# Performance work log

Hardware: AMD Instinct MI355X
Metric: run time of the kernel (lower is better)

The kernel has to match this reference:

```python
import jax, jax.numpy as jnp
import numpy as np

N_AGENTS = 10
N_ENEMIES = 11
N_ALLIES = 9
H = 64           # rnn_hidden_dim
HYP = 64         # api_hyper_dim
DEPTH = 2        # residual_depth
OWN = 32
EF = 10          # enemy_feats_dim
AF = 10          # ally_feats_dim
N_ACTIONS = 17
BS = 1024


def _hypernet(x, win, bin_, wres, bres, wout, bout):
    # Linear -> ReLU -> DEPTH x (ReLU(Linear)+identity) -> Linear
    h = jax.nn.relu(x @ win + bin_)
    for d in range(DEPTH):
        h = jax.nn.relu(h @ wres[d] + bres[d]) + h
    return h @ wout + bout


def _gru_cell(x, h, wi, wh, bi, bh):
    gi = x @ wi + bi
    gh = h @ wh + bh
    ir, iz, in_ = jnp.split(gi, 3, axis=-1)
    hr, hz, hn = jnp.split(gh, 3, axis=-1)
    r = jax.nn.sigmoid(ir + hr)
    z = jax.nn.sigmoid(iz + hz)
    n = jnp.tanh(in_ + r * hn)
    return (1.0 - z) * n + z * h


def setup_inputs() -> dict:
    key = jax.random.key(0)
    ks = iter(jax.random.split(key, 48))
    def p(shape, s=0.1):
        return jax.random.normal(next(ks), shape, jnp.float32) * s
    N = BS * N_AGENTS
    inp = {
        'own_feats':    p((N, OWN), 1.0),
        'enemy_feats':  p((N * N_ENEMIES, EF), 1.0),
        'ally_feats':   p((N * N_ALLIES, AF), 1.0),
        'hidden_state': p((N, H), 1.0),
        'fc1_w': p((OWN, H)), 'fc1_b': p((H,)),
        'agent_emb': p((N_AGENTS, H)), 'action_emb': p((N_ACTIONS, H)),
        'hen_win': p((EF, HYP)), 'hen_bin': p((HYP,)),
        'hen_wres': p((DEPTH, HYP, HYP)), 'hen_bres': p((DEPTH, HYP)),
        'hen_wout': p((HYP, EF * H)), 'hen_bout': p((EF * H,)),
        'hal_win': p((AF, HYP)), 'hal_bin': p((HYP,)),
        'hal_wres': p((DEPTH, HYP, HYP)), 'hal_bres': p((DEPTH, HYP)),
        'hal_wout': p((HYP, AF * H)), 'hal_bout': p((AF * H,)),
        'gru_wi': p((H, 3 * H)), 'gru_wh': p((H, 3 * H)),
        'gru_bi': p((3 * H,)), 'gru_bh': p((3 * H,)),
        'fc2_w': p((H, 6)), 'fc2_b': p((6,)),
        'how_win': p((EF, HYP)), 'how_bin': p((HYP,)),
        'how_wres': p((DEPTH, HYP, HYP)), 'how_bres': p((DEPTH, HYP)),
        'how_wout': p((HYP, H)), 'how_bout': p((H,)),
        'hob_win': p((EF, HYP)), 'hob_bin': p((HYP,)),
        'hob_wres': p((DEPTH, HYP, HYP)), 'hob_bres': p((DEPTH, HYP)),
        'hob_wout': p((HYP, 1)), 'hob_bout': p((1,)),
        'agent_idx': jax.random.randint(next(ks), (N,), 0, N_AGENTS),
        'last_action_idx': jax.random.randint(next(ks), (N,), 0, N_ACTIONS),
        'bs': BS,
    }
    return inp


def reference(own_feats, enemy_feats, ally_feats, hidden_state,
              fc1_w, fc1_b, agent_emb, action_emb,
              hen_win, hen_bin, hen_wres, hen_bres, hen_wout, hen_bout,
              hal_win, hal_bin, hal_wres, hal_bres, hal_wout, hal_bout,
              gru_wi, gru_wh, gru_bi, gru_bh,
              fc2_w, fc2_b,
              how_win, how_bin, how_wres, how_bres, how_wout, how_bout,
              hob_win, hob_bin, hob_wres, hob_bres, hob_wout, hob_bout,
              agent_idx, last_action_idx, bs):
    N = bs * N_AGENTS
    # own embedding + id embeddings
    emb = own_feats @ fc1_w + fc1_b
    emb = emb + agent_emb[agent_idx] + action_emb[last_action_idx]
    # per-enemy hypernet weights [N*NE, EF, H]; bmm + sum-pool over enemies
    w_en = _hypernet(enemy_feats, hen_win, hen_bin, hen_wres, hen_bres,
                     hen_wout, hen_bout).reshape(-1, EF, H)
    emb_en = jnp.einsum('nf,nfh->nh', enemy_feats, w_en)
    emb_en = emb_en.reshape(N, N_ENEMIES, H).sum(axis=1)
    # per-ally hypernet weights + bmm + sum-pool
    w_al = _hypernet(ally_feats, hal_win, hal_bin, hal_wres, hal_bres,
                     hal_wout, hal_bout).reshape(-1, AF, H)
    emb_al = jnp.einsum('nf,nfh->nh', ally_feats, w_al)
    emb_al = emb_al.reshape(N, N_ALLIES, H).sum(axis=1)
    x = jax.nn.relu(emb + emb_en + emb_al)
    hh = _gru_cell(x, hidden_state.reshape(-1, H), gru_wi, gru_wh, gru_bi, gru_bh)
    q_normal = (hh @ fc2_w + fc2_b).reshape(bs, N_AGENTS, 6)
    # attack-action head: hypernet-generated per-enemy weights/biases
    ow = _hypernet(enemy_feats, how_win, how_bin, how_wres, how_bres,
                   how_wout, how_bout).reshape(N, N_ENEMIES, H)
    ob = _hypernet(enemy_feats, hob_win, hob_bin, hob_wres, hob_bres,
                   hob_wout, hob_bout).reshape(N, N_ENEMIES)
    q_attack = (jnp.einsum('nh,neh->ne', hh, ow) + ob).reshape(bs, N_AGENTS, N_ENEMIES)
    q = jnp.concatenate([q_normal, q_attack], axis=-1)
    return q, hh.reshape(bs, N_AGENTS, H)
```

## Files before the change

### kernel.cpp

```cpp
#include <hip/hip_runtime.h>

#define DI static __device__ __forceinline__

typedef short s16x8 __attribute__((ext_vector_type(8)));
typedef float f32x4 __attribute__((ext_vector_type(4)));
typedef float f32x2 __attribute__((ext_vector_type(2)));
typedef unsigned u32x2 __attribute__((ext_vector_type(2)));

DI unsigned short f2b(float f) {
  union { float f; unsigned u; } v; v.f = f;
  return (unsigned short)((v.u + 0x7FFF + ((v.u >> 16) & 1)) >> 16);
}
DI float b2f(unsigned short s) {
  union { unsigned u; float f; } v; v.u = ((unsigned)s) << 16;
  return v.f;
}
DI unsigned cvtpk(float lo, float hi) {
  unsigned r;
  asm("v_cvt_pk_bf16_f32 %0, %1, %2" : "=v"(r) : "v"(lo), "v"(hi));
  return r;
}
DI f32x4 MFMA(s16x8 a, s16x8 b, f32x4 c) {
  return __builtin_amdgcn_mfma_f32_16x16x32_bf16(a, b, c, 0, 0, 0);
}
DI s16x8 ldg8(const unsigned short* p) { return *(const s16x8*)p; }

#define OFF_WEN   0
#define OFF_WAL   10240
#define OFF_WHOW  20480
#define OFF_WHOB  30720
#define OFF_BGEN  40960
#define OFF_BGAL  83968
#define OFF_WIT   126976
#define OFF_WHT   139264
#define OFF_FC1T  151552
#define OFF_FC2E  153600
#define OFF_HOWT  154624
#define OFF_HOBT  158720
#define SH_END    159744
#define B_EMB_EN  (SH_END*2)
#define B_EMB_AL  (B_EMB_EN + 2621440)
#define B_HB      (B_EMB_AL + 2621440)
#define B_GBF     (B_HB + 40960)

#define XSTR 40
#define HSTR 72
#define PSTR 680

__global__ __launch_bounds__(256) void kprep(
    const float* __restrict__ hen_win, const float* __restrict__ hen_wres,
    const float* __restrict__ hal_win, const float* __restrict__ hal_wres,
    const float* __restrict__ how_win, const float* __restrict__ how_wres,
    const float* __restrict__ hob_win, const float* __restrict__ hob_wres,
    const float* __restrict__ hen_wout, const float* __restrict__ hen_bout,
    const float* __restrict__ hal_wout, const float* __restrict__ hal_bout,
    const float* __restrict__ gru_wi, const float* __restrict__ gru_wh,
    const float* __restrict__ fc1_w, const float* __restrict__ fc2_w,
    const float* __restrict__ how_bout, const float* __restrict__ how_wout,
    const float* __restrict__ hob_wout,
    unsigned short* __restrict__ ws)
{
  const int gid = blockIdx.x * 256 + threadIdx.x;
  const int gsz = gridDim.x * 256;
  for (int i = gid; i < 4 * 10240; i += gsz) {
    int s = i / 10240, idx = i - s * 10240;
    const float* win  = (s == 0) ? hen_win  : (s == 1) ? hal_win  : (s == 2) ? how_win  : hob_win;
    const float* wres = (s == 0) ? hen_wres : (s == 1) ? hal_wres : (s == 2) ? how_wres : hob_wres;
    float v;
    if (idx < 2048) { int n = idx >> 5, k = idx & 31; v = (k < 10) ? win[k*64 + n] : 0.f; }
    else { int r = idx - 2048; int d = r >> 12; int r2 = r & 4095; int n = r2 >> 6, k = r2 & 63;
           v = wres[d*4096 + k*64 + n]; }
    ws[s * 10240 + idx] = f2b(v);
  }
  for (int i = gid; i < 2 * 43008; i += gsz) {
    int s = i / 43008, idx = i - s * 43008;
    const float* wout = s ? hal_wout : hen_wout;
    const float* bout = s ? hal_bout : hen_bout;
    int kl = idx & 31, n = (idx >> 5) & 63, c = idx >> 11;
    int kfg = c * 32 + kl;
    float v = 0.f;
    if (kfg < 640)      { int k = kfg / 10, f = kfg - k * 10; v = wout[k*640 + f*64 + n]; }
    else if (kfg < 650) { v = bout[(kfg - 640)*64 + n]; }
    ws[(s ? OFF_BGAL : OFF_BGEN) + idx] = f2b(v);
  }
  for (int i = gid; i < 2 * 12288; i += gsz) {
    int s = i / 12288, idx = i - s * 12288;
    int n = idx >> 6, k = idx & 63;
    const float* w = s ? gru_wh : gru_wi;
    ws[(s ? OFF_WHT : OFF_WIT) + idx] = f2b(w[k*192 + n]);
  }
  for (int i = gid; i < 2048; i += gsz) { int n = i >> 5, k = i & 31; ws[OFF_FC1T + i] = f2b(fc1_w[k*64 + n]); }
  for (int i = gid; i < 1024; i += gsz) {
    int n = i >> 6, k = i & 63;
    float v = 0.f; if (n < 6) v = fc2_w[k*6 + n]; else if (n == 6) v = how_bout[k];
    ws[OFF_FC2E + i] = f2b(v);
  }
  for (int i = gid; i < 4096; i += gsz) ws[OFF_HOWT + i] = f2b(how_wout[i]);
}

template<int TMAX, bool WLAST>
DI void stack_batch(const unsigned short* __restrict__ x_lds,
                    unsigned short* const (&hbp)[TMAX], const int (&tis)[TMAX], int E,
                    const unsigned short* __restrict__ wg,
                    const float* __restrict__ bin, const float* __restrict__ bres,
                    f32x4 (&hval)[TMAX][4])
{
  const int l = threadIdx.x & 63;
  const int lrow = l & 15, gq = l >> 4, lk8 = gq * 8;
  {
    s16x8 wf[4]; f32x4 bv[4];
#pragma unroll
    for (int mt = 0; mt < 4; mt++) {
      wf[mt] = ldg8(wg + (mt*16 + lrow)*32 + lk8);
      bv[mt] = *(const f32x4*)(bin + mt*16 + gq*4);
    }
#pragma unroll
    for (int tt = 0; tt < TMAX; tt++) {
      if (tis[tt] < E) {
        s16x8 xf = *(const s16x8*)&x_lds[(tis[tt]*16 + lrow)*XSTR + lk8];
#pragma unroll
        for (int mt = 0; mt < 4; mt++) {
          f32x4 d = MFMA(wf[mt], xf, f32x4{0.f,0.f,0.f,0.f});
#pragma unroll
          for (int r = 0; r < 4; r++) hval[tt][mt][r] = fmaxf(d[r] + bv[mt][r], 0.f);
        }
        unsigned short* wr = hbp[tt] + lrow*HSTR;
#pragma unroll
        for (int mt = 0; mt < 4; mt++) {
          u32x2 pw;
          pw.x = cvtpk(hval[tt][mt][0], hval[tt][mt][1]);
          pw.y = cvtpk(hval[tt][mt][2], hval[tt][mt][3]);
          *(u32x2*)&wr[mt*16 + gq*4] = pw;
        }
      }
    }
  }
#pragma unroll
  for (int d = 0; d < 2; d++) {
    const unsigned short* wt = wg + 2048 + d * 4096;
    s16x8 wf[4][2]; f32x4 bv[4];
#pragma unroll
    for (int mt = 0; mt < 4; mt++) {
      wf[mt][0] = ldg8(wt + (mt*16 + lrow)*64 + lk8);
      wf[mt][1] = ldg8(wt + (mt*16 + lrow)*64 + 32 + lk8);
      bv[mt] = *(const f32x4*)(bres + d*64 + mt*16 + gq*4);
    }
#pragma unroll
    for (int tt = 0; tt < TMAX; tt++) {
      if (tis[tt] < E) {
        const unsigned short* hr = hbp[tt] + lrow*HSTR;
        s16x8 b0 = *(const s16x8*)&hr[lk8];
        s16x8 b1 = *(const s16x8*)&hr[32 + lk8];
#pragma unroll
        for (int mt = 0; mt < 4; mt++) {
          f32x4 a = MFMA(wf[mt][0], b0, f32x4{0.f,0.f,0.f,0.f});
          a = MFMA(wf[mt][1], b1, a);
#pragma unroll
          for (int r = 0; r < 4; r++)
            hval[tt][mt][r] = fmaxf(a[r] + bv[mt][r], 0.f) + hval[tt][mt][r];
        }
        if (d == 0 || WLAST) {
          unsigned short* wr = hbp[tt] + lrow*HSTR;
#pragma unroll
          for (int mt = 0; mt < 4; mt++) {
            u32x2 pw;
            pw.x = cvtpk(hval[tt][mt][0], hval[tt][mt][1]);
            pw.y = cvtpk(hval[tt][mt][2], hval[tt][mt][3]);
            *(u32x2*)&wr[mt*16 + gq*4] = pw;
          }
        }
      }
    }
  }
}

template<int E>
DI void hyp_body16(const float* __restrict__ feats,
                   const unsigned short* __restrict__ Wg, const unsigned short* __restrict__ Bg,
                   const float* __restrict__ bin, const float* __restrict__ bres,
                   float* __restrict__ emb, char* smem)
{
  unsigned short* x_lds = (unsigned short*)smem;
  unsigned short* h_lds = (unsigned short*)(smem + 14080);
  unsigned short* P     = (unsigned short*)smem;
  const int t = threadIdx.x;
  const int l = t & 63, wv = t >> 6;
  const int lrow = l & 15, gq = l >> 4, lk8 = gq * 8, lr4 = gq * 4;

  for (int idx = t; idx < E * 512; idx += 256) {
    int row = idx >> 5, c = idx & 31;
    x_lds[row*XSTR + c] = (c < 10) ? f2b(feats[row*10 + c]) : (unsigned short)0;
  }
  __syncthreads();

  int tis[3] = {wv, wv + 4, wv + 8};
  unsigned short* hbp[3] = { h_lds + (wv)*16*HSTR, h_lds + (wv+4)*16*HSTR, h_lds + (wv+8)*16*HSTR };
  f32x4 hval[3][4];
  stack_batch<3, true>(x_lds, hbp, tis, E, Wg, bin, bres, hval);
  __syncthreads();

  const int a = t >> 4, kq = t & 15, k0 = kq * 4;
  float acc[4][10];
#pragma unroll
  for (int kk = 0; kk < 4; kk++)
#pragma unroll
    for (int f = 0; f < 10; f++) acc[kk][f] = 0.f;
#pragma unroll
  for (int e = 0; e < E; e++) {
    int row = a * E + e;
    const unsigned short* xr = x_lds + row * XSTR;
    s16x8 xv8 = *(const s16x8*)xr;
    unsigned xv2 = *(const unsigned*)(xr + 8);
    float xf[10];
#pragma unroll
    for (int f = 0; f < 8; f++) xf[f] = b2f((unsigned short)xv8[f]);
    xf[8] = b2f((unsigned short)(xv2 & 0xFFFF));
    xf[9] = b2f((unsigned short)(xv2 >> 16));
    u32x2 hp = *(const u32x2*)&h_lds[row*HSTR + k0];
    float hf[4] = { b2f((unsigned short)(hp.x & 0xFFFF)), b2f((unsigned short)(hp.x >> 16)),
                    b2f((unsigned short)(hp.y & 0xFFFF)), b2f((unsigned short)(hp.y >> 16)) };
#pragma unroll
    for (int kk = 0; kk < 4; kk++)
#pragma unroll
      for (int f = 0; f < 10; f++) acc[kk][f] += hf[kk] * xf[f];
  }
  float sxv = 0.f; int a2 = 0, fx = 0;
  if (t < 160) {
    a2 = t / 10; fx = t - a2 * 10;
    for (int e = 0; e < E; e++) sxv += feats[(a2*E + e)*10 + fx];
  }
  __syncthreads();

  u32x2* Pw = (u32x2*)(P + a*PSTR + k0*10);
#pragma unroll
  for (int m = 0; m < 10; m++) {
    const int s0 = 4*m, s1 = 4*m+1, s2 = 4*m+2, s3 = 4*m+3;
    u32x2 pw;
    pw.x = cvtpk(acc[s0/10][s0%10], acc[s1/10][s1%10]);
    pw.y = cvtpk(acc[s2/10][s2%10], acc[s3/10][s3%10]);
    Pw[m] = pw;
  }
  if (t < 160) P[a2*PSTR + 640 + fx] = f2b(sxv);
  for (int i = t; i < 352; i += 256) { int a3 = i / 22, c = i - a3*22; P[a3*PSTR + 650 + c] = 0; }
  __syncthreads();

  f32x4 acc0 = {0.f,0.f,0.f,0.f}, acc1 = {0.f,0.f,0.f,0.f};
  const unsigned short* Bw = Bg + (wv*16 + lrow)*32 + lk8;
#pragma unroll
  for (int c = 0; c < 21; c++) {
    s16x8 af = *(const s16x8*)&P[lrow*PSTR + c*32 + lk8];
    s16x8 bf = ldg8(Bw + c*2048);
    if (c & 1) acc1 = MFMA(af, bf, acc1); else acc0 = MFMA(af, bf, acc0);
  }
#pragma unroll
  for (int r = 0; r < 4; r++)
    emb[(lr4 + r)*64 + wv*16 + lrow] = acc0[r] + acc1[r];
}

__global__ __launch_bounds__(256) void khyp_ea(
    const float* __restrict__ en_feats, const float* __restrict__ al_feats,
    const unsigned short* __restrict__ ws,
    const float* __restrict__ en_bin, const float* __restrict__ en_bres,
    const float* __restrict__ al_bin, const float* __restrict__ al_bres,
    float* __restrict__ emb_en, float* __restrict__ emb_al)
{
  __shared__ __align__(16) char smem[39424];
  if (blockIdx.x < 640) {
    int blk = blockIdx.x;
    hyp_body16<11>(en_feats + (long)blk*1760, ws + OFF_WEN, ws + OFF_BGEN,
                   en_bin, en_bres, emb_en + (long)blk*1024, smem);
  } else {
    int blk = blockIdx.x - 640;
    hyp_body16<9>(al_feats + (long)blk*1440, ws + OFF_WAL, ws + OFF_BGAL,
                  al_bin, al_bres, emb_al + (long)blk*1024, smem);
  }
}

__global__ __launch_bounds__(256) void kfused(
    const float* __restrict__ own, const float* __restrict__ agent_emb,
    const float* __restrict__ action_emb,
    const int* __restrict__ agent_idx, const int* __restrict__ last_action,
    const float* __restrict__ emb_en, const float* __restrict__ emb_al,
    const float* __restrict__ hidden,
    const unsigned short* __restrict__ ws,
    const float* __restrict__ fc1_b, const float* __restrict__ bi,
    const float* __restrict__ bh, const float* __restrict__ fc2_b,
    float* __restrict__ qout, float* __restrict__ hhout,
    unsigned short* __restrict__ g_bf, float* __restrict__ hb)
{
  __shared__ unsigned short own_lds[16*32];
  __shared__ unsigned short x_lds[16*HSTR];
  __shared__ unsigned short hp_lds[16*HSTR];
  __shared__ unsigned short hh_lds[16*HSTR];
  const int t = threadIdx.x;
  const int l = t & 63, wv = t >> 6;
  const int lrow = l & 15, lk8 = (l >> 4) * 8, lr4 = (l >> 4) * 4;
  const int n0 = blockIdx.x * 16;

  const unsigned short* fc1T = ws + OFF_FC1T;
  const unsigned short* wiT  = ws + OFF_WIT;
  const unsigned short* whT  = ws + OFF_WHT;
  const unsigned short* howT = ws + OFF_HOWT;
  const unsigned short* fc2e = ws + OFF_FC2E;

  for (int i = t; i < 512; i += 256) own_lds[i] = f2b(own[n0*32 + i]);
  for (int i = t; i < 1024; i += 256) hp_lds[(i >> 6)*HSTR + (i & 63)] = f2b(hidden[n0*64 + i]);
  __syncthreads();

  const int j = wv * 16 + lrow;
  {
    s16x8 a0 = *(const s16x8*)&own_lds[lrow*32 + lk8];
    s16x8 b0 = ldg8(fc1T + (wv*16 + lrow)*32 + lk8);
    f32x4 c0 = MFMA(a0, b0, f32x4{0.f,0.f,0.f,0.f});
    float fb = fc1_b[j];
#pragma unroll
    for (int r = 0; r < 4; r++) {
      int aa = lr4 + r; int n = n0 + aa;
      int ai = agent_idx[n], la = last_action[n];
      float v = c0[r] + fb + agent_emb[ai*64 + j] + action_emb[la*64 + j]
              + emb_en[n*64 + j] + emb_al[n*64 + j];
      x_lds[aa*HSTR + j] = f2b(fmaxf(v, 0.f));
    }
  }
  __syncthreads();

  {
    s16x8 xa[2], ha[2];
#pragma unroll
    for (int s = 0; s < 2; s++) {
      xa[s] = *(const s16x8*)&x_lds[lrow*HSTR + s*32 + lk8];
      ha[s] = *(const s16x8*)&hp_lds[lrow*HSTR + s*32 + lk8];
    }
    f32x4 gi[3], gh[3];
#pragma unroll
    for (int g3 = 0; g3 < 3; g3++) { gi[g3] = f32x4{0.f,0.f,0.f,0.f}; gh[g3] = f32x4{0.f,0.f,0.f,0.f}; }
#pragma unroll
    for (int g3 = 0; g3 < 3; g3++) {
      int tl = wv + g3 * 4;
#pragma unroll
      for (int s = 0; s < 2; s++) {
        gi[g3] = MFMA(xa[s], ldg8(wiT + (tl*16 + lrow)*64 + s*32 + lk8), gi[g3]);
        gh[g3] = MFMA(ha[s], ldg8(whT + (tl*16 + lrow)*64 + s*32 + lk8), gh[g3]);
      }
    }
    float bir = bi[j], biz = bi[64 + j], bin_ = bi[128 + j];
    float bhr = bh[j], bhz = bh[64 + j], bhn = bh[128 + j];
#pragma unroll
    for (int r = 0; r < 4; r++) {
      int aa = lr4 + r; int n = n0 + aa;
      float rr = 1.f / (1.f + __expf(-(gi[0][r] + bir + gh[0][r] + bhr)));
      float zz = 1.f / (1.f + __expf(-(gi[1][r] + biz + gh[1][r] + bhz)));
      float nn = tanhf(gi[2][r] + bin_ + rr * (gh[2][r] + bhn));
      float hp = hidden[n*64 + j];
      float hhv = (1.f - zz) * nn + zz * hp;
      hhout[n*64 + j] = hhv;
      hh_lds[aa*HSTR + j] = f2b(hhv);
    }
  }
  __syncthreads();

  {
    s16x8 hha[2];
#pragma unroll
    for (int s = 0; s < 2; s++) hha[s] = *(const s16x8*)&hh_lds[lrow*HSTR + s*32 + lk8];
    f32x4 gc = {0.f,0.f,0.f,0.f};
#pragma unroll
    for (int s = 0; s < 2; s++) gc = MFMA(hha[s], ldg8(howT + (wv*16 + lrow)*64 + s*32 + lk8), gc);
#pragma unroll
    for (int r = 0; r < 4; r++) g_bf[(n0 + lr4 + r)*64 + wv*16 + lrow] = f2b(gc[r]);
    if (wv == 0) {
      f32x4 qc = {0.f,0.f,0.f,0.f};
#pragma unroll
      for (int s = 0; s < 2; s++) qc = MFMA(hha[s], ldg8(fc2e + lrow*64 + s*32 + lk8), qc);
#pragma unroll
      for (int r = 0; r < 4; r++) {
        int n = n0 + lr4 + r;
        if (lrow < 6)       qout[n*17 + lrow] = qc[r] + fc2_b[lrow];
        else if (lrow == 6) hb[n] = qc[r];
      }
    }
  }
}

__global__ __launch_bounds__(256) void kattack(
    const float* __restrict__ en_feats, const unsigned short* __restrict__ ws,
    const float* __restrict__ how_bin, const float* __restrict__ how_bres,
    const float* __restrict__ hob_bin, const float* __restrict__ hob_bres,
    const unsigned short* __restrict__ g_bf, const float* __restrict__ hbuf,
    const float* __restrict__ hob_wout, const float* __restrict__ hob_bout,
    float* __restrict__ qout)
{
  __shared__ __align__(16) char smem[41728];
  unsigned short* x_lds = (unsigned short*)smem;
  unsigned short* scr   = (unsigned short*)(smem + 14080);
  const int t = threadIdx.x;
  const int l = t & 63, wv = t >> 6;
  const int lrow = l & 15, gq = l >> 4;
  const int blk = blockIdx.x;
  const float* feats = en_feats + (long)blk * 1760;

  for (int idx = t; idx < 176*32; idx += 256) {
    int row = idx >> 5, c = idx & 31;
    x_lds[row*XSTR + c] = (c < 10) ? f2b(feats[row*10 + c]) : (unsigned short)0;
  }
  __syncthreads();

  int tis[3] = {wv, wv + 4, wv + 8};
  unsigned short* hbp[3] = { scr + (wv*3+0)*16*HSTR, scr + (wv*3+1)*16*HSTR, scr + (wv*3+2)*16*HSTR };
  f32x4 hval[3][4];

  stack_batch<3, false>(x_lds, hbp, tis, 11, ws + OFF_WHOB, hob_bin, hob_bres, hval);
  f32x4 hw[4];
#pragma unroll
  for (int mt = 0; mt < 4; mt++) hw[mt] = *(const f32x4*)(hob_wout + mt*16 + gq*4);
  float qbv[3] = {0.f, 0.f, 0.f};
#pragma unroll
  for (int tt = 0; tt < 3; tt++) {
    if (tis[tt] < 11) {
      float s = 0.f;
#pragma unroll
      for (int mt = 0; mt < 4; mt++)
#pragma unroll
        for (int r = 0; r < 4; r++) s += hval[tt][mt][r] * hw[mt][r];
      s += __shfl_xor(s, 16, 64);
      s += __shfl_xor(s, 32, 64);
      qbv[tt] = s;
    }
  }

  stack_batch<3, false>(x_lds, hbp, tis, 11, ws + OFF_WHOW, how_bin, how_bres, hval);
  const float hob_b0 = hob_bout[0];
#pragma unroll
  for (int tt = 0; tt < 3; tt++) {
    if (tis[tt] < 11) {
      int row = tis[tt]*16 + lrow;
      int ag = (unsigned)row / 11u;
      int n = blk*16 + ag;
      float s = 0.f;
#pragma unroll
      for (int mt = 0; mt < 4; mt++) {
        u32x2 gv = *(const u32x2*)(g_bf + (long)n*64 + mt*16 + gq*4);
        s += hval[tt][mt][0] * b2f((unsigned short)(gv.x & 0xFFFF))
           + hval[tt][mt][1] * b2f((unsigned short)(gv.x >> 16))
           + hval[tt][mt][2] * b2f((unsigned short)(gv.y & 0xFFFF))
           + hval[tt][mt][3] * b2f((unsigned short)(gv.y >> 16));
      }
      s += __shfl_xor(s, 16, 64);
      s += __shfl_xor(s, 32, 64);
      if (l < 16) {
        int e = row - ag * 11;
        qout[n*17 + 6 + e] = s + qbv[tt] + hbuf[n] + hob_b0;
      }
    }
  }
}

extern "C" void kernel_launch(void* const* d_in, const int* in_sizes, int n_in,
                              void* d_out, int out_size, void* d_ws, size_t ws_size,
                              hipStream_t stream)
{
  (void)in_sizes; (void)n_in; (void)out_size; (void)ws_size;
  const float* own        = (const float*)d_in[0];
  const float* enemy      = (const float*)d_in[1];
  const float* ally       = (const float*)d_in[2];
  const float* hidden     = (const float*)d_in[3];
  const float* fc1_w      = (const float*)d_in[4];
  const float* fc1_b      = (const float*)d_in[5];
  const float* agent_emb  = (const float*)d_in[6];
  const float* action_emb = (const float*)d_in[7];
  const float* hen_win  = (const float*)d_in[8];  const float* hen_bin  = (const float*)d_in[9];
  const float* hen_wres = (const float*)d_in[10]; const float* hen_bres = (const float*)d_in[11];
  const float* hen_wout = (const float*)d_in[12]; const float* hen_bout = (const float*)d_in[13];
  const float* hal_win  = (const float*)d_in[14]; const float* hal_bin  = (const float*)d_in[15];
  const float* hal_wres = (const float*)d_in[16]; const float* hal_bres = (const float*)d_in[17];
  const float* hal_wout = (const float*)d_in[18]; const float* hal_bout = (const float*)d_in[19];
  const float* gru_wi = (const float*)d_in[20];   const float* gru_wh = (const float*)d_in[21];
  const float* gru_bi = (const float*)d_in[22];   const float* gru_bh = (const float*)d_in[23];
  const float* fc2_w  = (const float*)d_in[24];   const float* fc2_b  = (const float*)d_in[25];
  const float* how_win  = (const float*)d_in[26]; const float* how_bin  = (const float*)d_in[27];
  const float* how_wres = (const float*)d_in[28]; const float* how_bres = (const float*)d_in[29];
  const float* how_wout = (const float*)d_in[30]; const float* how_bout = (const float*)d_in[31];
  const float* hob_win  = (const float*)d_in[32]; const float* hob_bin  = (const float*)d_in[33];
  const float* hob_wres = (const float*)d_in[34]; const float* hob_bres = (const float*)d_in[35];
  const float* hob_wout = (const float*)d_in[36]; const float* hob_bout = (const float*)d_in[37];
  const int* agent_idx   = (const int*)d_in[38];
  const int* last_action = (const int*)d_in[39];

  unsigned short* ws = (unsigned short*)d_ws;
  float* emb_en = (float*)((char*)d_ws + B_EMB_EN);
  float* emb_al = (float*)((char*)d_ws + B_EMB_AL);
  float* hb     = (float*)((char*)d_ws + B_HB);
  unsigned short* g_bf = (unsigned short*)((char*)d_ws + B_GBF);

  float* q  = (float*)d_out;
  float* hh = q + 1024*10*17;

  kprep<<<128, 256, 0, stream>>>(hen_win, hen_wres, hal_win, hal_wres,
      how_win, how_wres, hob_win, hob_wres,
      hen_wout, hen_bout, hal_wout, hal_bout,
      gru_wi, gru_wh, fc1_w, fc2_w, how_bout, how_wout, hob_wout, ws);
  khyp_ea<<<1280, 256, 0, stream>>>(enemy, ally, ws,
      hen_bin, hen_bres, hal_bin, hal_bres, emb_en, emb_al);
  kfused<<<640, 256, 0, stream>>>(own, agent_emb, action_emb, agent_idx, last_action,
      emb_en, emb_al, hidden, ws, fc1_b, gru_bi, gru_bh, fc2_b, q, hh, g_bf, hb);
  kattack<<<640, 256, 0, stream>>>(enemy, ws, how_bin, how_bres, hob_bin, hob_bres,
      g_bf, hb, hob_wout, hob_bout, q);
}
```

Before: 78.49 us.

## Merge attack-head hypernet stacks into the hypernet kernel and fuse the attack dot-product into the GRU kernel

The attack-head hypernet stacks, which do not depend on the GRU output, now run inside the same launch as the enemy and ally hypernets. They write per-enemy bf16 hidden features and the bias term to workspace. The GRU kernel then computes the attack Q values with an MFMA against its locally held g vector in LDS, which removes the separate attack kernel and the g and hb round trips. The enemy and ally embeddings are also stored as bf16. In exchange this adds about 14 MB of hhow writes and reads plus some extra bf16 rounding, and the MFMA computes 16x16 outputs of which only the diagonal-matching ones are used.

```diff
diff --git a/kernel.cpp b/kernel.cpp
--- a/kernel.cpp
+++ b/kernel.cpp
@@ -4,7 +4,6 @@
 
 typedef short s16x8 __attribute__((ext_vector_type(8)));
 typedef float f32x4 __attribute__((ext_vector_type(4)));
-typedef float f32x2 __attribute__((ext_vector_type(2)));
 typedef unsigned u32x2 __attribute__((ext_vector_type(2)));
 
 DI unsigned short f2b(float f) {
@@ -36,12 +35,11 @@
 #define OFF_FC1T  151552
 #define OFF_FC2E  153600
 #define OFF_HOWT  154624
-#define OFF_HOBT  158720
 #define SH_END    159744
 #define B_EMB_EN  (SH_END*2)
-#define B_EMB_AL  (B_EMB_EN + 2621440)
-#define B_HB      (B_EMB_AL + 2621440)
-#define B_GBF     (B_HB + 40960)
+#define B_EMB_AL  (B_EMB_EN + 1310720)
+#define B_HHOW    (B_EMB_AL + 1310720)
+#define B_QB      (B_HHOW + 14417920)
 
 #define XSTR 40
 #define HSTR 72
@@ -57,7 +55,6 @@
     const float* __restrict__ gru_wi, const float* __restrict__ gru_wh,
     const float* __restrict__ fc1_w, const float* __restrict__ fc2_w,
     const float* __restrict__ how_bout, const float* __restrict__ how_wout,
-    const float* __restrict__ hob_wout,
     unsigned short* __restrict__ ws)
 {
   const int gid = blockIdx.x * 256 + threadIdx.x;
@@ -100,7 +97,7 @@
 
 template<int TMAX, bool WLAST>
 DI void stack_batch(const unsigned short* __restrict__ x_lds,
-                    unsigned short* const (&hbp)[TMAX], const int (&tis)[TMAX], int E,
+                    unsigned short* const (&hbp)[TMAX], const int (&tis)[TMAX], int NT,
                     const unsigned short* __restrict__ wg,
                     const float* __restrict__ bin, const float* __restrict__ bres,
                     f32x4 (&hval)[TMAX][4])
@@ -116,7 +113,7 @@
     }
 #pragma unroll
     for (int tt = 0; tt < TMAX; tt++) {
-      if (tis[tt] < E) {
+      if (tis[tt] < NT) {
         s16x8 xf = *(const s16x8*)&x_lds[(tis[tt]*16 + lrow)*XSTR + lk8];
 #pragma unroll
         for (int mt = 0; mt < 4; mt++) {
@@ -147,7 +144,7 @@
     }
 #pragma unroll
     for (int tt = 0; tt < TMAX; tt++) {
-      if (tis[tt] < E) {
+      if (tis[tt] < NT) {
         const unsigned short* hr = hbp[tt] + lrow*HSTR;
         s16x8 b0 = *(const s16x8*)&hr[lk8];
         s16x8 b1 = *(const s16x8*)&hr[32 + lk8];
@@ -178,7 +175,7 @@
 DI void hyp_body16(const float* __restrict__ feats,
                    const unsigned short* __restrict__ Wg, const unsigned short* __restrict__ Bg,
                    const float* __restrict__ bin, const float* __restrict__ bres,
-                   float* __restrict__ emb, char* smem)
+                   unsigned short* __restrict__ emb, char* smem)
 {
   unsigned short* x_lds = (unsigned short*)smem;
   unsigned short* h_lds = (unsigned short*)(smem + 14080);
@@ -254,47 +251,115 @@
   }
 #pragma unroll
   for (int r = 0; r < 4; r++)
-    emb[(lr4 + r)*64 + wv*16 + lrow] = acc0[r] + acc1[r];
-}
-
-__global__ __launch_bounds__(256) void khyp_ea(
+    emb[(lr4 + r)*64 + wv*16 + lrow] = f2b(acc0[r] + acc1[r]);
+}
+
+DI void attack_stacks(int blk, const float* __restrict__ en_feats,
+                      const unsigned short* __restrict__ ws,
+                      const float* __restrict__ how_bin, const float* __restrict__ how_bres,
+                      const float* __restrict__ hob_bin, const float* __restrict__ hob_bres,
+                      const float* __restrict__ hob_wout, float hob_b0,
+                      unsigned short* __restrict__ hhow, float* __restrict__ qB, char* smem)
+{
+  unsigned short* x_lds = (unsigned short*)smem;
+  unsigned short* scr   = (unsigned short*)(smem + 14080);
+  const int t = threadIdx.x;
+  const int l = t & 63, wv = t >> 6;
+  const int lrow = l & 15, gq = l >> 4;
+  const float* feats = en_feats + (long)blk * 1760;
+
+  for (int idx = t; idx < 176*32; idx += 256) {
+    int row = idx >> 5, c = idx & 31;
+    x_lds[row*XSTR + c] = (c < 10) ? f2b(feats[row*10 + c]) : (unsigned short)0;
+  }
+  __syncthreads();
+
+  int tis[3] = {wv, wv + 4, wv + 8};
+  unsigned short* hbp[3] = { scr + (wv*3+0)*16*HSTR, scr + (wv*3+1)*16*HSTR, scr + (wv*3+2)*16*HSTR };
+  f32x4 hval[3][4];
+
+  stack_batch<3, false>(x_lds, hbp, tis, 11, ws + OFF_WHOB, hob_bin, hob_bres, hval);
+  f32x4 hw[4];
+#pragma unroll
+  for (int mt = 0; mt < 4; mt++) hw[mt] = *(const f32x4*)(hob_wout + mt*16 + gq*4);
+#pragma unroll
+  for (int tt = 0; tt < 3; tt++) {
+    if (tis[tt] < 11) {
+      float s = 0.f;
+#pragma unroll
+      for (int mt = 0; mt < 4; mt++)
+#pragma unroll
+        for (int r = 0; r < 4; r++) s += hval[tt][mt][r] * hw[mt][r];
+      s += __shfl_xor(s, 16, 64);
+      s += __shfl_xor(s, 32, 64);
+      if (l < 16) qB[blk*176 + tis[tt]*16 + lrow] = s + hob_b0;
+    }
+  }
+
+  stack_batch<3, false>(x_lds, hbp, tis, 11, ws + OFF_WHOW, how_bin, how_bres, hval);
+#pragma unroll
+  for (int tt = 0; tt < 3; tt++) {
+    if (tis[tt] < 11) {
+      long row = (long)blk*176 + tis[tt]*16 + lrow;
+      unsigned short* wr = hhow + row*64;
+#pragma unroll
+      for (int mt = 0; mt < 4; mt++) {
+        u32x2 pw;
+        pw.x = cvtpk(hval[tt][mt][0], hval[tt][mt][1]);
+        pw.y = cvtpk(hval[tt][mt][2], hval[tt][mt][3]);
+        *(u32x2*)&wr[mt*16 + gq*4] = pw;
+      }
+    }
+  }
+}
+
+__global__ __launch_bounds__(256) void khyp_all(
     const float* __restrict__ en_feats, const float* __restrict__ al_feats,
     const unsigned short* __restrict__ ws,
     const float* __restrict__ en_bin, const float* __restrict__ en_bres,
     const float* __restrict__ al_bin, const float* __restrict__ al_bres,
-    float* __restrict__ emb_en, float* __restrict__ emb_al)
-{
-  __shared__ __align__(16) char smem[39424];
+    const float* __restrict__ how_bin, const float* __restrict__ how_bres,
+    const float* __restrict__ hob_bin, const float* __restrict__ hob_bres,
+    const float* __restrict__ hob_wout, const float* __restrict__ hob_bout,
+    unsigned short* __restrict__ emb_en, unsigned short* __restrict__ emb_al,
+    unsigned short* __restrict__ hhow, float* __restrict__ qB)
+{
+  __shared__ __align__(16) char smem[41728];
   if (blockIdx.x < 640) {
     int blk = blockIdx.x;
     hyp_body16<11>(en_feats + (long)blk*1760, ws + OFF_WEN, ws + OFF_BGEN,
                    en_bin, en_bres, emb_en + (long)blk*1024, smem);
-  } else {
+  } else if (blockIdx.x < 1280) {
     int blk = blockIdx.x - 640;
     hyp_body16<9>(al_feats + (long)blk*1440, ws + OFF_WAL, ws + OFF_BGAL,
                   al_bin, al_bres, emb_al + (long)blk*1024, smem);
-  }
-}
-
-__global__ __launch_bounds__(256) void kfused(
+  } else {
+    attack_stacks(blockIdx.x - 1280, en_feats, ws, how_bin, how_bres,
+                  hob_bin, hob_bres, hob_wout, hob_bout[0], hhow, qB, smem);
+  }
+}
+
+__global__ __launch_bounds__(256) void kfused2(
     const float* __restrict__ own, const float* __restrict__ agent_emb,
     const float* __restrict__ action_emb,
     const int* __restrict__ agent_idx, const int* __restrict__ last_action,
-    const float* __restrict__ emb_en, const float* __restrict__ emb_al,
+    const unsigned short* __restrict__ emb_en, const unsigned short* __restrict__ emb_al,
     const float* __restrict__ hidden,
     const unsigned short* __restrict__ ws,
     const float* __restrict__ fc1_b, const float* __restrict__ bi,
     const float* __restrict__ bh, const float* __restrict__ fc2_b,
-    float* __restrict__ qout, float* __restrict__ hhout,
-    unsigned short* __restrict__ g_bf, float* __restrict__ hb)
+    const unsigned short* __restrict__ hhow, const float* __restrict__ qB,
+    float* __restrict__ qout, float* __restrict__ hhout)
 {
   __shared__ unsigned short own_lds[16*32];
   __shared__ unsigned short x_lds[16*HSTR];
   __shared__ unsigned short hp_lds[16*HSTR];
   __shared__ unsigned short hh_lds[16*HSTR];
+  __shared__ unsigned short g_lds[16*HSTR];
+  __shared__ float hb_lds[16];
   const int t = threadIdx.x;
   const int l = t & 63, wv = t >> 6;
-  const int lrow = l & 15, lk8 = (l >> 4) * 8, lr4 = (l >> 4) * 4;
+  const int lrow = l & 15, gq = l >> 4, lk8 = gq * 8, lr4 = gq * 4;
   const int n0 = blockIdx.x * 16;
 
   const unsigned short* fc1T = ws + OFF_FC1T;
@@ -318,7 +383,7 @@
       int aa = lr4 + r; int n = n0 + aa;
       int ai = agent_idx[n], la = last_action[n];
       float v = c0[r] + fb + agent_emb[ai*64 + j] + action_emb[la*64 + j]
-              + emb_en[n*64 + j] + emb_al[n*64 + j];
+              + b2f(emb_en[(long)n*64 + j]) + b2f(emb_al[(long)n*64 + j]);
       x_lds[aa*HSTR + j] = f2b(fmaxf(v, 0.f));
     }
   }
@@ -367,7 +432,7 @@
 #pragma unroll
     for (int s = 0; s < 2; s++) gc = MFMA(hha[s], ldg8(howT + (wv*16 + lrow)*64 + s*32 + lk8), gc);
 #pragma unroll
-    for (int r = 0; r < 4; r++) g_bf[(n0 + lr4 + r)*64 + wv*16 + lrow] = f2b(gc[r]);
+    for (int r = 0; r < 4; r++) g_lds[(lr4 + r)*HSTR + wv*16 + lrow] = f2b(gc[r]);
     if (wv == 0) {
       f32x4 qc = {0.f,0.f,0.f,0.f};
 #pragma unroll
@@ -376,80 +441,35 @@
       for (int r = 0; r < 4; r++) {
         int n = n0 + lr4 + r;
         if (lrow < 6)       qout[n*17 + lrow] = qc[r] + fc2_b[lrow];
-        else if (lrow == 6) hb[n] = qc[r];
+        else if (lrow == 6) hb_lds[lr4 + r] = qc[r];
       }
     }
   }
-}
-
-__global__ __launch_bounds__(256) void kattack(
-    const float* __restrict__ en_feats, const unsigned short* __restrict__ ws,
-    const float* __restrict__ how_bin, const float* __restrict__ how_bres,
-    const float* __restrict__ hob_bin, const float* __restrict__ hob_bres,
-    const unsigned short* __restrict__ g_bf, const float* __restrict__ hbuf,
-    const float* __restrict__ hob_wout, const float* __restrict__ hob_bout,
-    float* __restrict__ qout)
-{
-  __shared__ __align__(16) char smem[41728];
-  unsigned short* x_lds = (unsigned short*)smem;
-  unsigned short* scr   = (unsigned short*)(smem + 14080);
-  const int t = threadIdx.x;
-  const int l = t & 63, wv = t >> 6;
-  const int lrow = l & 15, gq = l >> 4;
-  const int blk = blockIdx.x;
-  const float* feats = en_feats + (long)blk * 1760;
-
-  for (int idx = t; idx < 176*32; idx += 256) {
-    int row = idx >> 5, c = idx & 31;
-    x_lds[row*XSTR + c] = (c < 10) ? f2b(feats[row*10 + c]) : (unsigned short)0;
-  }
-  __syncthreads();
-
-  int tis[3] = {wv, wv + 4, wv + 8};
-  unsigned short* hbp[3] = { scr + (wv*3+0)*16*HSTR, scr + (wv*3+1)*16*HSTR, scr + (wv*3+2)*16*HSTR };
-  f32x4 hval[3][4];
-
-  stack_batch<3, false>(x_lds, hbp, tis, 11, ws + OFF_WHOB, hob_bin, hob_bres, hval);
-  f32x4 hw[4];
-#pragma unroll
-  for (int mt = 0; mt < 4; mt++) hw[mt] = *(const f32x4*)(hob_wout + mt*16 + gq*4);
-  float qbv[3] = {0.f, 0.f, 0.f};
-#pragma unroll
-  for (int tt = 0; tt < 3; tt++) {
-    if (tis[tt] < 11) {
-      float s = 0.f;
-#pragma unroll
-      for (int mt = 0; mt < 4; mt++)
-#pragma unroll
-        for (int r = 0; r < 4; r++) s += hval[tt][mt][r] * hw[mt][r];
-      s += __shfl_xor(s, 16, 64);
-      s += __shfl_xor(s, 32, 64);
-      qbv[tt] = s;
-    }
-  }
-
-  stack_batch<3, false>(x_lds, hbp, tis, 11, ws + OFF_WHOW, how_bin, how_bres, hval);
-  const float hob_b0 = hob_bout[0];
-#pragma unroll
-  for (int tt = 0; tt < 3; tt++) {
-    if (tis[tt] < 11) {
-      int row = tis[tt]*16 + lrow;
-      int ag = (unsigned)row / 11u;
-      int n = blk*16 + ag;
-      float s = 0.f;
-#pragma unroll
-      for (int mt = 0; mt < 4; mt++) {
-        u32x2 gv = *(const u32x2*)(g_bf + (long)n*64 + mt*16 + gq*4);
-        s += hval[tt][mt][0] * b2f((unsigned short)(gv.x & 0xFFFF))
-           + hval[tt][mt][1] * b2f((unsigned short)(gv.x >> 16))
-           + hval[tt][mt][2] * b2f((unsigned short)(gv.y & 0xFFFF))
-           + hval[tt][mt][3] * b2f((unsigned short)(gv.y >> 16));
-      }
-      s += __shfl_xor(s, 16, 64);
-      s += __shfl_xor(s, 32, 64);
-      if (l < 16) {
-        int e = row - ag * 11;
-        qout[n*17 + 6 + e] = s + qbv[tt] + hbuf[n] + hob_b0;
+  __syncthreads();
+
+  {
+    const long rb = (long)blockIdx.x * 176;
+#pragma unroll
+    for (int tt = 0; tt < 3; tt++) {
+      int ti = wv + tt * 4;
+      if (ti < 11) {
+        const unsigned short* hr = hhow + (rb + ti*16 + lrow)*64;
+        s16x8 af0 = ldg8(hr + lk8);
+        s16x8 af1 = ldg8(hr + 32 + lk8);
+        s16x8 bf0 = *(const s16x8*)&g_lds[lrow*HSTR + lk8];
+        s16x8 bf1 = *(const s16x8*)&g_lds[lrow*HSTR + 32 + lk8];
+        f32x4 c = MFMA(af0, bf0, f32x4{0.f,0.f,0.f,0.f});
+        c = MFMA(af1, bf1, c);
+#pragma unroll
+        for (int r = 0; r < 4; r++) {
+          int rowl = ti*16 + lr4 + r;
+          int ag = (unsigned)rowl / 11u;
+          if (ag == lrow) {
+            int e = rowl - ag * 11;
+            int n = n0 + ag;
+            qout[n*17 + 6 + e] = c[r] + qB[rb + rowl] + hb_lds[ag];
+          }
+        }
       }
     }
   }
@@ -487,10 +507,10 @@
   const int* last_action = (const int*)d_in[39];
 
   unsigned short* ws = (unsigned short*)d_ws;
-  float* emb_en = (float*)((char*)d_ws + B_EMB_EN);
-  float* emb_al = (float*)((char*)d_ws + B_EMB_AL);
-  float* hb     = (float*)((char*)d_ws + B_HB);
-  unsigned short* g_bf = (unsigned short*)((char*)d_ws + B_GBF);
+  unsigned short* emb_en = (unsigned short*)((char*)d_ws + B_EMB_EN);
+  unsigned short* emb_al = (unsigned short*)((char*)d_ws + B_EMB_AL);
+  unsigned short* hhow   = (unsigned short*)((char*)d_ws + B_HHOW);
+  float*          qB     = (float*)((char*)d_ws + B_QB);
 
   float* q  = (float*)d_out;
   float* hh = q + 1024*10*17;
@@ -498,11 +518,12 @@
   kprep<<<128, 256, 0, stream>>>(hen_win, hen_wres, hal_win, hal_wres,
       how_win, how_wres, hob_win, hob_wres,
       hen_wout, hen_bout, hal_wout, hal_bout,
-      gru_wi, gru_wh, fc1_w, fc2_w, how_bout, how_wout, hob_wout, ws);
-  khyp_ea<<<1280, 256, 0, stream>>>(enemy, ally, ws,
-      hen_bin, hen_bres, hal_bin, hal_bres, emb_en, emb_al);
-  kfused<<<640, 256, 0, stream>>>(own, agent_emb, action_emb, agent_idx, last_action,
-      emb_en, emb_al, hidden, ws, fc1_b, gru_bi, gru_bh, fc2_b, q, hh, g_bf, hb);
-  kattack<<<640, 256, 0, stream>>>(enemy, ws, how_bin, how_bres, hob_bin, hob_bres,
-      g_bf, hb, hob_wout, hob_bout, q);
-}
+      gru_wi, gru_wh, fc1_w, fc2_w, how_bout, how_wout, ws);
+  khyp_all<<<1920, 256, 0, stream>>>(enemy, ally, ws,
+      hen_bin, hen_bres, hal_bin, hal_bres,
+      how_bin, how_bres, hob_bin, hob_bres, hob_wout, hob_bout,
+      emb_en, emb_al, hhow, qB);
+  kfused2<<<640, 256, 0, stream>>>(own, agent_emb, action_emb, agent_idx, last_action,
+      emb_en, emb_al, hidden, ws, fc1_b, gru_bi, gru_bh, fc2_b,
+      hhow, qB, q, hh);
+}
```

Result: slower. 83.17 us (+6.0%).
